# Optimization experiments

Measured on AMD Instinct MI355X. Metric: run time of the kernel, lower is better.

The kernel has to match this reference:

```python
import jax, jax.numpy as jnp
import numpy as np

N_CHANNELS = 64
# Static leave-one-out index table: row c lists all channels != c. Shape [C, C-1].
_LOO_IDX = np.array([[j for j in range(N_CHANNELS) if j != c] for c in range(N_CHANNELS)], dtype=np.int32)


def setup_inputs() -> dict:
    key = jax.random.key(0)
    kx, kw = jax.random.split(key)
    B, S, C = 4, 8192, N_CHANNELS
    x = jax.random.normal(kx, (B, S, C, 2), dtype=jnp.float32)
    # Stacked weights of the C Linear(2*(C-1) -> 2, bias=False) layers: [C, 2, 2*(C-1)].
    fan_in = 2 * (C - 1)
    bound = 1.0 / np.sqrt(fan_in)
    W = jax.random.uniform(kw, (C, 2, fan_in), dtype=jnp.float32, minval=-bound, maxval=bound)
    return {"x": x, "W": W}


def reference(x, W):
    # x: [B, S, C, 2] (real/imag), W: [C, 2, 2*(C-1)]
    idx = jnp.asarray(_LOO_IDX)                      # [C, C-1]
    amp = x[..., 0] ** 2 + x[..., 1] ** 2            # [B, S, C]
    distorted = amp[..., None] * x                   # [B, S, C, 2]
    fr = distorted[..., 0]                           # [B, S, C]
    fi = distorted[..., 1]                           # [B, S, C]
    # Leave-one-out gather for every target channel c: [B, S, C, C-1]
    fr_loo = fr[..., idx]
    fi_loo = fi[..., idx]
    total = jnp.concatenate([fr_loo, fi_loo], axis=-1)  # [B, S, C, 2*(C-1)]
    # Per-channel tiny linear, batched across B, S, C in one einsum.
    out = jnp.einsum('bscn,con->bsco', total, W)         # [B, S, C, 2]
    return out
```

## Files before the change

### kernel.cpp

```cpp
#include <hip/hip_runtime.h>


typedef _Float16 f16x8 __attribute__((ext_vector_type(8)));
typedef _Float16 f16x2 __attribute__((ext_vector_type(2)));
typedef float    floatx4 __attribute__((ext_vector_type(4)));

#define NPOS 32768
#define PT   4
#define TILE (16 * PT)
#define NBLK (NPOS / TILE)
#define MS   136

__global__ __launch_bounds__(256, 2)
void leakage_kernel(const float* __restrict__ x,
                    const float* __restrict__ W,
                    float* __restrict__ out) {
    __shared__ __align__(16) _Float16 Mt[128][MS];
    __shared__ __align__(16) _Float16 fsh[TILE][MS];

    const int tid  = threadIdx.x;
    const int w    = tid >> 6;
    const int lane = tid & 63;
    const int q    = lane >> 4, r = lane & 15;

#pragma unroll
    for (int it = 0; it < 16; ++it) {
        const int g = tid + 256 * it;
        if (g < 4032) {
            const float4 v = ((const float4*)W)[g];
#pragma unroll
            for (int u = 0; u < 4; ++u) {
                const int F  = 4 * g + u;
                const int n  = F / 126;
                const int m  = F - 126 * n;
                const int c  = n >> 1;
                const int mh = (m < 63) ? m : (m - 63);
                const int ch = mh + (mh >= c ? 1 : 0);
                const int k  = (m < 63) ? ch : (64 + ch);
                const float val = (u == 0) ? v.x : (u == 1) ? v.y
                                : (u == 2) ? v.z : v.w;
                Mt[n][k] = (_Float16)val;
            }
        }
    }
    if (tid < 128) {
        const int c = tid >> 1;
        Mt[tid][c]      = (_Float16)0.f;
        Mt[tid][64 + c] = (_Float16)0.f;
    }

    const int pbase = blockIdx.x * TILE;
    const float4* __restrict__ x4 = (const float4*)x + (size_t)pbase * 32;
#pragma unroll
    for (int it = 0; it < 2 * PT; ++it) {
        const int g = tid + 256 * it;
        const int p = g >> 5;
        const int i = g & 31;
        const float4 v = x4[g];
        const float a0 = v.x * v.x + v.y * v.y;
        const float a1 = v.z * v.z + v.w * v.w;
        f16x2 fr = { (_Float16)(a0 * v.x), (_Float16)(a1 * v.z) };
        f16x2 fi = { (_Float16)(a0 * v.y), (_Float16)(a1 * v.w) };
        *(f16x2*)&fsh[p][2 * i]      = fr;
        *(f16x2*)&fsh[p][64 + 2 * i] = fi;
    }
    __syncthreads();

    const int nt0 = 2 * w, nt1 = 2 * w + 1;
    f16x8 B0[4], B1[4];
#pragma unroll
    for (int t = 0; t < 4; ++t) {
        B0[t] = *(const f16x8*)&Mt[nt0 * 16 + r][32 * t + 8 * q];
        B1[t] = *(const f16x8*)&Mt[nt1 * 16 + r][32 * t + 8 * q];
    }

#pragma unroll
    for (int pt = 0; pt < PT; ++pt) {
        const int pr = pt * 16 + r;
        f16x8 A0 = *(const f16x8*)&fsh[pr][      8 * q];
        f16x8 A1 = *(const f16x8*)&fsh[pr][32 +  8 * q];
        f16x8 A2 = *(const f16x8*)&fsh[pr][64 +  8 * q];
        f16x8 A3 = *(const f16x8*)&fsh[pr][96 +  8 * q];

        floatx4 C0 = {0.f, 0.f, 0.f, 0.f};
        floatx4 C1 = {0.f, 0.f, 0.f, 0.f};
        C0 = __builtin_amdgcn_mfma_f32_16x16x32_f16(A0, B0[0], C0, 0, 0, 0);
        C1 = __builtin_amdgcn_mfma_f32_16x16x32_f16(A0, B1[0], C1, 0, 0, 0);
        C0 = __builtin_amdgcn_mfma_f32_16x16x32_f16(A1, B0[1], C0, 0, 0, 0);
        C1 = __builtin_amdgcn_mfma_f32_16x16x32_f16(A1, B1[1], C1, 0, 0, 0);
        C0 = __builtin_amdgcn_mfma_f32_16x16x32_f16(A2, B0[2], C0, 0, 0, 0);
        C1 = __builtin_amdgcn_mfma_f32_16x16x32_f16(A2, B1[2], C1, 0, 0, 0);
        C0 = __builtin_amdgcn_mfma_f32_16x16x32_f16(A3, B0[3], C0, 0, 0, 0);
        C1 = __builtin_amdgcn_mfma_f32_16x16x32_f16(A3, B1[3], C1, 0, 0, 0);

        float* __restrict__ op = out + (size_t)(pbase + pt * 16) * 128;
#pragma unroll
        for (int reg = 0; reg < 4; ++reg) {
            const int m = q * 4 + reg;
            op[(size_t)m * 128 + nt0 * 16 + r] = C0[reg];
            op[(size_t)m * 128 + nt1 * 16 + r] = C1[reg];
        }
    }
}

extern "C" void kernel_launch(void* const* d_in, const int* in_sizes, int n_in,
                              void* d_out, int out_size, void* d_ws, size_t ws_size,
                              hipStream_t stream) {
    const float* x = (const float*)d_in[0];
    const float* W = (const float*)d_in[1];
    float* out = (float*)d_out;

    hipLaunchKernelGGL(leakage_kernel, dim3(NBLK), dim3(256), 0, stream,
                       x, W, out);
}
```

Measured before the change: 74.41 us.

## Use 512-thread blocks covering two position chunks to amortize weight setup

Blocks grow to 512 threads with eight waves, and each wave now owns one 16-column output tile instead of two. Each block handles 128 positions in two sequential 64-position chunks, so the per-block weight-matrix build in shared memory is amortized over twice as many positions and half as many blocks are launched. The weight load is rewritten to use float2 reads with simpler index math. In exchange, chunks are processed serially behind extra barriers with no overlap of loads and compute, and the larger block size may reduce occupancy.

```diff
diff --git a/kernel.cpp b/kernel.cpp
--- a/kernel.cpp
+++ b/kernel.cpp
@@ -5,41 +5,42 @@
 typedef _Float16 f16x2 __attribute__((ext_vector_type(2)));
 typedef float    floatx4 __attribute__((ext_vector_type(4)));
 
-#define NPOS 32768
-#define PT   4
-#define TILE (16 * PT)
-#define NBLK (NPOS / TILE)
-#define MS   136
+#define NPOS  32768
+#define CPOS  64
+#define NCH   2
+#define BPOS  (CPOS * NCH)
+#define NBLK  (NPOS / BPOS)
+#define NTHR  512
+#define MS    136
 
-__global__ __launch_bounds__(256, 2)
+__global__ __launch_bounds__(NTHR, 2)
 void leakage_kernel(const float* __restrict__ x,
                     const float* __restrict__ W,
                     float* __restrict__ out) {
     __shared__ __align__(16) _Float16 Mt[128][MS];
-    __shared__ __align__(16) _Float16 fsh[TILE][MS];
+    __shared__ __align__(16) _Float16 fsh[CPOS][MS];
 
     const int tid  = threadIdx.x;
     const int w    = tid >> 6;
     const int lane = tid & 63;
     const int q    = lane >> 4, r = lane & 15;
 
+    const float2* __restrict__ W2 = (const float2*)W;
 #pragma unroll
     for (int it = 0; it < 16; ++it) {
-        const int g = tid + 256 * it;
-        if (g < 4032) {
-            const float4 v = ((const float4*)W)[g];
+        const int e  = tid + NTHR * it;
+        const int n  = e >> 6;
+        const int m2 = e & 63;
+        if (m2 < 63) {
+            const int c = n >> 1;
+            const float2 v = W2[n * 63 + m2];
 #pragma unroll
-            for (int u = 0; u < 4; ++u) {
-                const int F  = 4 * g + u;
-                const int n  = F / 126;
-                const int m  = F - 126 * n;
-                const int c  = n >> 1;
-                const int mh = (m < 63) ? m : (m - 63);
-                const int ch = mh + (mh >= c ? 1 : 0);
-                const int k  = (m < 63) ? ch : (64 + ch);
-                const float val = (u == 0) ? v.x : (u == 1) ? v.y
-                                : (u == 2) ? v.z : v.w;
-                Mt[n][k] = (_Float16)val;
+            for (int u = 0; u < 2; ++u) {
+                const int m    = 2 * m2 + u;
+                const int half = (m >= 63) ? 1 : 0;
+                const int mh   = m - 63 * half;
+                const int k    = 64 * half + mh + (mh >= c ? 1 : 0);
+                Mt[n][k] = (_Float16)(u == 0 ? v.x : v.y);
             }
         }
     }
@@ -49,56 +50,73 @@
         Mt[tid][64 + c] = (_Float16)0.f;
     }
 
-    const int pbase = blockIdx.x * TILE;
-    const float4* __restrict__ x4 = (const float4*)x + (size_t)pbase * 32;
+    const int pblk = blockIdx.x * BPOS;
+
+    {
+        const float4* __restrict__ x4 = (const float4*)x + (size_t)pblk * 32;
 #pragma unroll
-    for (int it = 0; it < 2 * PT; ++it) {
-        const int g = tid + 256 * it;
-        const int p = g >> 5;
-        const int i = g & 31;
-        const float4 v = x4[g];
-        const float a0 = v.x * v.x + v.y * v.y;
-        const float a1 = v.z * v.z + v.w * v.w;
-        f16x2 fr = { (_Float16)(a0 * v.x), (_Float16)(a1 * v.z) };
-        f16x2 fi = { (_Float16)(a0 * v.y), (_Float16)(a1 * v.w) };
-        *(f16x2*)&fsh[p][2 * i]      = fr;
-        *(f16x2*)&fsh[p][64 + 2 * i] = fi;
+        for (int it = 0; it < 4; ++it) {
+            const int g = tid + NTHR * it;
+            const int p = g >> 5;
+            const int i = g & 31;
+            const float4 v = x4[g];
+            const float a0 = v.x * v.x + v.y * v.y;
+            const float a1 = v.z * v.z + v.w * v.w;
+            *(f16x2*)&fsh[p][2 * i] =
+                f16x2{ (_Float16)(a0 * v.x), (_Float16)(a1 * v.z) };
+            *(f16x2*)&fsh[p][64 + 2 * i] =
+                f16x2{ (_Float16)(a0 * v.y), (_Float16)(a1 * v.w) };
+        }
     }
     __syncthreads();
 
-    const int nt0 = 2 * w, nt1 = 2 * w + 1;
-    f16x8 B0[4], B1[4];
-#pragma unroll
-    for (int t = 0; t < 4; ++t) {
-        B0[t] = *(const f16x8*)&Mt[nt0 * 16 + r][32 * t + 8 * q];
-        B1[t] = *(const f16x8*)&Mt[nt1 * 16 + r][32 * t + 8 * q];
-    }
+    f16x8 B0 = *(const f16x8*)&Mt[16 * w + r][ 0 + 8 * q];
+    f16x8 B1 = *(const f16x8*)&Mt[16 * w + r][32 + 8 * q];
+    f16x8 B2 = *(const f16x8*)&Mt[16 * w + r][64 + 8 * q];
+    f16x8 B3 = *(const f16x8*)&Mt[16 * w + r][96 + 8 * q];
 
 #pragma unroll
-    for (int pt = 0; pt < PT; ++pt) {
-        const int pr = pt * 16 + r;
-        f16x8 A0 = *(const f16x8*)&fsh[pr][      8 * q];
-        f16x8 A1 = *(const f16x8*)&fsh[pr][32 +  8 * q];
-        f16x8 A2 = *(const f16x8*)&fsh[pr][64 +  8 * q];
-        f16x8 A3 = *(const f16x8*)&fsh[pr][96 +  8 * q];
+    for (int ch = 0; ch < NCH; ++ch) {
+#pragma unroll
+        for (int pt = 0; pt < 4; ++pt) {
+            const int pr = pt * 16 + r;
+            f16x8 A0 = *(const f16x8*)&fsh[pr][ 0 + 8 * q];
+            f16x8 A1 = *(const f16x8*)&fsh[pr][32 + 8 * q];
+            f16x8 A2 = *(const f16x8*)&fsh[pr][64 + 8 * q];
+            f16x8 A3 = *(const f16x8*)&fsh[pr][96 + 8 * q];
 
-        floatx4 C0 = {0.f, 0.f, 0.f, 0.f};
-        floatx4 C1 = {0.f, 0.f, 0.f, 0.f};
-        C0 = __builtin_amdgcn_mfma_f32_16x16x32_f16(A0, B0[0], C0, 0, 0, 0);
-        C1 = __builtin_amdgcn_mfma_f32_16x16x32_f16(A0, B1[0], C1, 0, 0, 0);
-        C0 = __builtin_amdgcn_mfma_f32_16x16x32_f16(A1, B0[1], C0, 0, 0, 0);
-        C1 = __builtin_amdgcn_mfma_f32_16x16x32_f16(A1, B1[1], C1, 0, 0, 0);
-        C0 = __builtin_amdgcn_mfma_f32_16x16x32_f16(A2, B0[2], C0, 0, 0, 0);
-        C1 = __builtin_amdgcn_mfma_f32_16x16x32_f16(A2, B1[2], C1, 0, 0, 0);
-        C0 = __builtin_amdgcn_mfma_f32_16x16x32_f16(A3, B0[3], C0, 0, 0, 0);
-        C1 = __builtin_amdgcn_mfma_f32_16x16x32_f16(A3, B1[3], C1, 0, 0, 0);
+            floatx4 C = {0.f, 0.f, 0.f, 0.f};
+            C = __builtin_amdgcn_mfma_f32_16x16x32_f16(A0, B0, C, 0, 0, 0);
+            C = __builtin_amdgcn_mfma_f32_16x16x32_f16(A1, B1, C, 0, 0, 0);
+            C = __builtin_amdgcn_mfma_f32_16x16x32_f16(A2, B2, C, 0, 0, 0);
+            C = __builtin_amdgcn_mfma_f32_16x16x32_f16(A3, B3, C, 0, 0, 0);
 
-        float* __restrict__ op = out + (size_t)(pbase + pt * 16) * 128;
+            float* __restrict__ op =
+                out + (size_t)(pblk + ch * CPOS + pt * 16) * 128;
 #pragma unroll
-        for (int reg = 0; reg < 4; ++reg) {
-            const int m = q * 4 + reg;
-            op[(size_t)m * 128 + nt0 * 16 + r] = C0[reg];
-            op[(size_t)m * 128 + nt1 * 16 + r] = C1[reg];
+            for (int reg = 0; reg < 4; ++reg) {
+                op[(size_t)(4 * q + reg) * 128 + 16 * w + r] = C[reg];
+            }
+        }
+
+        if (ch + 1 < NCH) {
+            __syncthreads();
+            const float4* __restrict__ x4 =
+                (const float4*)x + (size_t)(pblk + (ch + 1) * CPOS) * 32;
+#pragma unroll
+            for (int it = 0; it < 4; ++it) {
+                const int g = tid + NTHR * it;
+                const int p = g >> 5;
+                const int i = g & 31;
+                const float4 v = x4[g];
+                const float a0 = v.x * v.x + v.y * v.y;
+                const float a1 = v.z * v.z + v.w * v.w;
+                *(f16x2*)&fsh[p][2 * i] =
+                    f16x2{ (_Float16)(a0 * v.x), (_Float16)(a1 * v.z) };
+                *(f16x2*)&fsh[p][64 + 2 * i] =
+                    f16x2{ (_Float16)(a0 * v.y), (_Float16)(a1 * v.w) };
+            }
+            __syncthreads();
         }
     }
 }
@@ -110,6 +128,6 @@
     const float* W = (const float*)d_in[1];
     float* out = (float*)d_out;
 
-    hipLaunchKernelGGL(leakage_kernel, dim3(NBLK), dim3(256), 0, stream,
+    hipLaunchKernelGGL(leakage_kernel, dim3(NBLK), dim3(NTHR), 0, stream,
                        x, W, out);
 }
```

Measured after the change: 72.20 us. 3.0% less time.
